# Performance work log

Hardware: AMD Instinct MI355X
Metric: run time of the kernel (lower is better)

The kernel has to match this reference:

```python
import jax, jax.numpy as jnp
import numpy as np

NUM_PRODUCTS = 100000
NUM_CATEGORIES = 1000
P_DIM = 64          # product embedding dim
C_DIM = P_DIM // 2  # 32
T_DIM = P_DIM // 4  # 16
U_DIM = P_DIM // 4  # 16
HID = 128
B, S, L = 1024, 50, 20


def setup_inputs() -> dict:
    key = jax.random.key(0)
    ks = jax.random.split(key, 24)
    inp = {}
    inp['product_input'] = jax.random.randint(ks[0], (B, S, L), 1, NUM_PRODUCTS + 1, dtype=jnp.int32)
    inp['categories_input'] = jax.random.randint(ks[1], (B, S, L), 1, NUM_CATEGORIES + 1, dtype=jnp.int32)
    inp['user_age_input'] = jax.random.uniform(ks[2], (B,), jnp.float32) * 80.0
    inp['user_timestamps_input'] = jax.random.uniform(ks[3], (B, S), jnp.float32)
    inp['user_gender_input'] = jax.random.randint(ks[4], (B,), 0, 2).astype(jnp.float32)
    # embedding tables (padding_idx=0 -> zero row)
    emb_p = jax.random.normal(ks[5], (NUM_PRODUCTS + 1, P_DIM), jnp.float32) * 0.02
    inp['emb_p'] = emb_p.at[0].set(0.0)
    emb_c = jax.random.normal(ks[6], (NUM_CATEGORIES + 1, C_DIM), jnp.float32) * 0.02
    inp['emb_c'] = emb_c.at[0].set(0.0)
    # small linears
    inp['W_ts'] = jax.random.normal(ks[7], (T_DIM, 1), jnp.float32) * 0.1
    inp['b_ts'] = jnp.zeros((T_DIM,), jnp.float32)
    inp['W_uf'] = jax.random.normal(ks[8], (U_DIM, 2), jnp.float32) * 0.1
    inp['b_uf'] = jnp.zeros((U_DIM,), jnp.float32)
    # 2-layer LSTM params (torch layout: [4H, in], gate order i,f,g,o)
    IN = P_DIM + C_DIM + T_DIM + U_DIM  # 128
    sc = 1.0 / np.sqrt(HID)
    inp['W_ih0'] = jax.random.uniform(ks[9], (4 * HID, IN), jnp.float32, -sc, sc)
    inp['W_hh0'] = jax.random.uniform(ks[10], (4 * HID, HID), jnp.float32, -sc, sc)
    inp['b_ih0'] = jax.random.uniform(ks[11], (4 * HID,), jnp.float32, -sc, sc)
    inp['b_hh0'] = jax.random.uniform(ks[12], (4 * HID,), jnp.float32, -sc, sc)
    inp['W_ih1'] = jax.random.uniform(ks[13], (4 * HID, HID), jnp.float32, -sc, sc)
    inp['W_hh1'] = jax.random.uniform(ks[14], (4 * HID, HID), jnp.float32, -sc, sc)
    inp['b_ih1'] = jax.random.uniform(ks[15], (4 * HID,), jnp.float32, -sc, sc)
    inp['b_hh1'] = jax.random.uniform(ks[16], (4 * HID,), jnp.float32, -sc, sc)
    # MLP head
    inp['W1'] = jax.random.normal(ks[17], (HID // 2, HID), jnp.float32) * 0.05
    inp['b1'] = jnp.zeros((HID // 2,), jnp.float32)
    inp['W2'] = jax.random.normal(ks[18], (NUM_PRODUCTS + 1, HID // 2), jnp.float32) * 0.05
    inp['b2'] = jnp.zeros((NUM_PRODUCTS + 1,), jnp.float32)
    return inp


def _lstm_layer(x, Wih, Whh, bih, bhh):
    # x: [S, B, D] -> outputs [S, B, H], final h [B, H]
    Bb = x.shape[1]
    h0 = jnp.zeros((Bb, HID), x.dtype)
    def step(carry, xt):
        h, c = carry
        gates = xt @ Wih.T + bih + h @ Whh.T + bhh
        i, f, g, o = jnp.split(gates, 4, axis=-1)
        c = jax.nn.sigmoid(f) * c + jax.nn.sigmoid(i) * jnp.tanh(g)
        h = jax.nn.sigmoid(o) * jnp.tanh(c)
        return (h, c), h
    (h, c), ys = jax.lax.scan(step, (h0, h0), x)
    return ys, h


def reference(product_input, categories_input, user_age_input, user_timestamps_input,
              user_gender_input, emb_p, emb_c, W_ts, b_ts, W_uf, b_uf,
              W_ih0, W_hh0, b_ih0, b_hh0, W_ih1, W_hh1, b_ih1, b_hh1,
              W1, b1, W2, b2):
    # per-basket mean-pooled embeddings (fused gather + segment mean)
    prod = emb_p[product_input].mean(axis=2)          # [B, S, 64]
    cat = emb_c[categories_input].mean(axis=2)        # [B, S, 32]
    ts = user_timestamps_input[..., None] @ W_ts.T + b_ts  # [B, S, 16]
    uf = jnp.stack([user_age_input, user_gender_input], axis=1) @ W_uf.T + b_uf  # [B, 16]
    uf = jnp.broadcast_to(uf[:, None, :], (uf.shape[0], prod.shape[1], uf.shape[1]))
    x = jnp.concatenate([prod, cat, ts, uf], axis=-1)  # [B, S, 128]
    x = jnp.transpose(x, (1, 0, 2))                    # [S, B, 128]
    ys0, _ = _lstm_layer(x, W_ih0, W_hh0, b_ih0, b_hh0)
    _, h_last = _lstm_layer(ys0, W_ih1, W_hh1, b_ih1, b_hh1)  # [B, H]
    # dropout is identity in eval mode
    hidden = jax.nn.relu(h_last @ W1.T + b1)
    logits = hidden @ W2.T + b2                        # [B, num_products+1]
    return logits
```

## Files before the change

### kernel.cpp

```cpp
#include <hip/hip_runtime.h>

#define B_    1024
#define S_    50
#define L_    20
#define NOUT  100001

typedef __attribute__((ext_vector_type(8))) short bh8;
typedef __attribute__((ext_vector_type(4))) float fx4;

__device__ __forceinline__ unsigned short f2bf(float x){
  unsigned u = __float_as_uint(x);
  unsigned r = (u + 0x7FFFu + ((u >> 16) & 1u)) >> 16;
  return (unsigned short)r;
}
__device__ __forceinline__ float bf2f(unsigned short h){
  return __uint_as_float(((unsigned)h) << 16);
}
__device__ __forceinline__ float sigm(float x){
  return __builtin_amdgcn_rcpf(1.f + __expf(-x));
}
__device__ __forceinline__ float tanh_(float x){
  return 1.f - 2.f*__builtin_amdgcn_rcpf(__expf(2.f*x) + 1.f);
}

__device__ __forceinline__ void frag_convert_row(const float* src, bh8& hv, bh8& lv){
  #pragma unroll
  for (int j = 0; j < 8; j++){
    float x = src[j];
    unsigned short hb = f2bf(x);
    hv[j] = (short)hb;
    lv[j] = (short)f2bf(x - bf2f(hb));
  }
}

__global__ __launch_bounds__(256) void prep_lstm_w(
    const float* __restrict__ Wih0, const float* __restrict__ Whh0,
    const float* __restrict__ bih0, const float* __restrict__ bhh0,
    const float* __restrict__ Wih1, const float* __restrict__ Whh1,
    const float* __restrict__ bih1, const float* __restrict__ bhh1,
    short* __restrict__ wsw, float* __restrict__ wsbias){
  int tid = blockIdx.x*256 + threadIdx.x;
  if (tid < 1024){
    int l = tid >> 9, n = tid & 511;
    wsbias[l*512 + n] = l ? (bih1[n] + bhh1[n]) : (bih0[n] + bhh0[n]);
  }
  if (tid >= 32768) return;
  int lane = tid & 63;
  int kt   = (tid >> 6) & 7;
  int nt   = (tid >> 9) & 31;
  int l    = tid >> 14;
  const float* Wih = l ? Wih1 : Wih0;
  const float* Whh = l ? Whh1 : Whh0;
  int n = nt*16 + (lane & 15);
  int kbase = kt*32 + (lane >> 4)*8;
  size_t base = ((((size_t)l*32 + nt)*8 + kt)*64 + lane)*8;
  for (int j = 0; j < 8; j++){
    int k = kbase + j;
    float w = (k < 128) ? Wih[n*128 + k] : Whh[n*128 + (k - 128)];
    wsw[base + j] = (short)f2bf(w);
  }
}

__global__ __launch_bounds__(256) void prep_w2(const float* __restrict__ W2,
                                               short* __restrict__ out){
  long i = (long)blockIdx.x*256 + threadIdx.x;
  if (i >= 100016L*64) return;
  long row = i >> 6;
  float v = (row < NOUT) ? W2[i] : 0.f;
  out[i] = (short)f2bf(v);
}

__global__ __launch_bounds__(256) void features(
    const int* __restrict__ pidx, const int* __restrict__ cidx,
    const float* __restrict__ age, const float* __restrict__ ts,
    const float* __restrict__ gender,
    const float* __restrict__ embp, const float* __restrict__ embc,
    const float* __restrict__ Wts, const float* __restrict__ bts,
    const float* __restrict__ Wuf, const float* __restrict__ bufv,
    short* __restrict__ xfrag){
  const int bx = blockIdx.x;
  const int bt = bx & 63, s = bx >> 6;
  const int b0 = bt*16;
  const int tid = threadIdx.x;
  __shared__ int pi[320], ci[320];
  __shared__ __align__(16) float XF[16][132];
  for (int i = tid; i < 640; i += 256){
    if (i < 320){
      int row = i/20, l = i - row*20;
      pi[i] = pidx[((size_t)(b0+row)*S_ + s)*L_ + l];
    } else {
      int j = i - 320;
      int row = j/20, l = j - row*20;
      ci[j] = cidx[((size_t)(b0+row)*S_ + s)*L_ + l];
    }
  }
  __syncthreads();
  const int m = tid >> 4, fg = tid & 15;
  float a[8];
  if (fg < 8){
    int f0 = fg*8;
    float4 s0 = {0,0,0,0}, s1 = {0,0,0,0};
    for (int l = 0; l < L_; l++){
      const float4* p = (const float4*)(embp + (size_t)pi[m*20+l]*64 + f0);
      float4 u = p[0], v = p[1];
      s0.x += u.x; s0.y += u.y; s0.z += u.z; s0.w += u.w;
      s1.x += v.x; s1.y += v.y; s1.z += v.z; s1.w += v.w;
    }
    a[0]=s0.x*0.05f; a[1]=s0.y*0.05f; a[2]=s0.z*0.05f; a[3]=s0.w*0.05f;
    a[4]=s1.x*0.05f; a[5]=s1.y*0.05f; a[6]=s1.z*0.05f; a[7]=s1.w*0.05f;
  } else if (fg < 12){
    int f0 = (fg-8)*8;
    float4 s0 = {0,0,0,0}, s1 = {0,0,0,0};
    for (int l = 0; l < L_; l++){
      const float4* p = (const float4*)(embc + (size_t)ci[m*20+l]*32 + f0);
      float4 u = p[0], v = p[1];
      s0.x += u.x; s0.y += u.y; s0.z += u.z; s0.w += u.w;
      s1.x += v.x; s1.y += v.y; s1.z += v.z; s1.w += v.w;
    }
    a[0]=s0.x*0.05f; a[1]=s0.y*0.05f; a[2]=s0.z*0.05f; a[3]=s0.w*0.05f;
    a[4]=s1.x*0.05f; a[5]=s1.y*0.05f; a[6]=s1.z*0.05f; a[7]=s1.w*0.05f;
  } else if (fg < 14){
    int j0 = (fg-12)*8;
    float tv = ts[(size_t)(b0+m)*S_ + s];
    #pragma unroll
    for (int e = 0; e < 8; e++) a[e] = tv*Wts[j0+e] + bts[j0+e];
  } else {
    int j0 = (fg-14)*8;
    float av = age[b0+m], gv = gender[b0+m];
    #pragma unroll
    for (int e = 0; e < 8; e++){
      int j = j0+e;
      a[e] = av*Wuf[2*j] + gv*Wuf[2*j+1] + bufv[j];
    }
  }
  {
    int f0 = fg*8;
    *(float4*)&XF[m][f0]   = (float4){a[0],a[1],a[2],a[3]};
    *(float4*)&XF[m][f0+4] = (float4){a[4],a[5],a[6],a[7]};
  }
  __syncthreads();
  const int kt = tid >> 6, ls = tid & 63;
  const int mm = ls & 15, a2 = ls >> 4;
  bh8 hv, lv;
  frag_convert_row(&XF[mm][kt*32 + a2*8], hv, lv);
  size_t ob = ((((size_t)s*64 + bt)*2 + 0)*4 + kt)*512 + (size_t)ls*8;
  *(bh8*)(xfrag + ob)        = hv;
  *(bh8*)(xfrag + ob + 2048) = lv;
}

__global__ __launch_bounds__(1024, 4) void lstm_kernel(
    const short* __restrict__ xfrag, const short* __restrict__ wsw,
    const float* __restrict__ wsbias,
    const float* __restrict__ W1, const float* __restrict__ b1,
    short* __restrict__ hidden_bf){
  __shared__ __align__(16) short XAhi[2][2048], XAlo[2][2048];
  __shared__ __align__(16) short H0hi[2][2048], H0lo[2][2048];
  __shared__ __align__(16) short H1hi[2][2048], H1lo[2][2048];
  __shared__ __align__(16) float XH0f[16][132], XH1f[16][132];
  const int tid  = threadIdx.x;
  const int w    = tid >> 6, lane = tid & 63;
  const int col  = lane & 15, quad = lane >> 4;
  const int bt   = blockIdx.x;
  const int u    = w & 7;
  const bool t1  = (w >= 8);
  const int lsel = t1 ? 1 : 0;
  const int pl2  = tid >> 9, sl2 = tid & 511;
  const bh8* wp = (const bh8*)wsw;

  for (int idx = tid; idx < 2048; idx += 1024){
    H0hi[1][idx] = 0; H0lo[1][idx] = 0;
    H1hi[0][idx] = 0; H1lo[0][idx] = 0;
  }
  float bz[4];
  #pragma unroll
  for (int g = 0; g < 4; g++)
    bz[g] = wsbias[lsel*512 + (g*8 + u)*16 + col];
  float cst[4] = {0,0,0,0};
  {
    float2 v = *(const float2*)(xfrag + ((size_t)bt*2 + pl2)*2048 + (size_t)sl2*4);
    *(float2*)((pl2 ? XAlo[0] : XAhi[0]) + sl2*4) = v;
  }
  __syncthreads();

  for (int i = 0; i <= S_; i++){
    const int cb = i & 1, pb = cb ^ 1;
    int tp = (i+1 < S_) ? i+1 : S_-1;
    float2 pf = *(const float2*)(xfrag + (((size_t)tp*64 + bt)*2 + pl2)*2048 + (size_t)sl2*4);

    const bool act = t1 ? (i >= 1) : (i < S_);
    if (act){
      fx4 acc[4];
      #pragma unroll
      for (int g = 0; g < 4; g++)
        acc[g] = (fx4){bz[g], bz[g], bz[g], bz[g]};
      __builtin_amdgcn_s_setprio(1);
      #pragma unroll
      for (int kt = 0; kt < 8; kt++){
        const short* ph;
        const short* pl;
        if (!t1){
          ph = (kt < 4) ? &XAhi[cb][kt*512 + lane*8] : &H0hi[pb][(kt-4)*512 + lane*8];
          pl = (kt < 4) ? &XAlo[cb][kt*512 + lane*8] : &H0lo[pb][(kt-4)*512 + lane*8];
        } else {
          ph = (kt < 4) ? &H0hi[pb][kt*512 + lane*8] : &H1hi[pb][(kt-4)*512 + lane*8];
          pl = (kt < 4) ? &H0lo[pb][kt*512 + lane*8] : &H1lo[pb][(kt-4)*512 + lane*8];
        }
        bh8 ah = *(const bh8*)ph;
        bh8 al = *(const bh8*)pl;
        #pragma unroll
        for (int g = 0; g < 4; g++){
          bh8 bb = wp[(size_t)((lsel*32 + g*8 + u)*8 + kt)*64 + lane];
          acc[g] = __builtin_amdgcn_mfma_f32_16x16x32_bf16(ah, bb, acc[g], 0, 0, 0);
          acc[g] = __builtin_amdgcn_mfma_f32_16x16x32_bf16(al, bb, acc[g], 0, 0, 0);
        }
      }
      __builtin_amdgcn_s_setprio(0);
      float (*XH)[132] = t1 ? XH1f : XH0f;
      #pragma unroll
      for (int r = 0; r < 4; r++){
        float cc = sigm(acc[1][r])*cst[r] + sigm(acc[0][r])*tanh_(acc[2][r]);
        cst[r] = cc;
        XH[quad*4 + r][u*16 + col] = sigm(acc[3][r])*tanh_(cc);
      }
      {
        const int mm = lane & 15, qq = (lane >> 4) & 1, phase = lane >> 5;
        bh8 hv, lv;
        frag_convert_row(&XH[mm][u*16 + qq*8], hv, lv);
        const int off = (u >> 1)*512 + ((2*(u & 1) + qq)*16 + mm)*8;
        short* dsth = t1 ? &H1hi[cb][off] : &H0hi[cb][off];
        short* dstl = t1 ? &H1lo[cb][off] : &H0lo[cb][off];
        short* dst  = phase ? dstl : dsth;
        bh8   val   = phase ? lv : hv;
        *(bh8*)dst = val;
      }
    }
    *(float2*)((pl2 ? XAlo[pb] : XAhi[pb]) + sl2*4) = pf;
    __syncthreads();
  }
  {
    const int mm2 = tid >> 6;
    const int cc2 = tid & 63;
    float s = b1[cc2];
    #pragma unroll 8
    for (int k = 0; k < 128; k++) s += XH1f[mm2][k]*W1[cc2*128 + k];
    s = fmaxf(s, 0.f);
    hidden_bf[(size_t)(bt*16 + mm2)*64 + cc2] = (short)f2bf(s);
  }
}

__global__ __launch_bounds__(256) void head2(
    const short* __restrict__ hid, const short* __restrict__ w2,
    const float* __restrict__ b2, float* __restrict__ out){
  __shared__ __align__(16) float HS[4][16][132];
  const int tid = threadIdx.x;
  const int w = tid >> 6, lane = tid & 63;
  const int col = lane & 15, quad = lane >> 4;
  const int mt = blockIdx.x & 63;
  const int chunk = blockIdx.x >> 6;
  const bh8* hp = (const bh8*)hid;
  bh8 a0 = hp[(size_t)(mt*16 + col)*8 + quad];
  bh8 a1 = hp[(size_t)(mt*16 + col)*8 + 4 + quad];
  const bh8* wpt = (const bh8*)w2;
  #pragma unroll
  for (int i = 0; i < 8; i++){
    int nt = chunk*32 + w*8 + i;
    if (nt < 6251){
      int n = nt*16 + col;
      bh8 b0v = wpt[(size_t)n*8 + quad];
      bh8 b1v = wpt[(size_t)n*8 + 4 + quad];
      fx4 a = {0.f,0.f,0.f,0.f};
      a = __builtin_amdgcn_mfma_f32_16x16x32_bf16(a0, b0v, a, 0, 0, 0);
      a = __builtin_amdgcn_mfma_f32_16x16x32_bf16(a1, b1v, a, 0, 0, 0);
      float bias = (n < NOUT) ? b2[n] : 0.f;
      #pragma unroll
      for (int r = 0; r < 4; r++) HS[w][quad*4 + r][i*16 + col] = a[r] + bias;
    }
  }
  __syncthreads();
  const long rowbase = (long)mt*16;
  const int n0 = chunk*512 + w*128;
  #pragma unroll
  for (int p = 0; p < 8; p++){
    int row = p*2 + (lane >> 5);
    int c4 = (lane & 31)*4;
    int gc = n0 + c4;
    float4 v = *(const float4*)&HS[w][row][c4];
    if (gc + 3 < NOUT){
      *(float4*)&out[(rowbase + row)*NOUT + gc] = v;
    } else {
      float vv[4] = {v.x, v.y, v.z, v.w};
      #pragma unroll
      for (int k2 = 0; k2 < 4; k2++)
        if (gc + k2 < NOUT) out[(rowbase + row)*NOUT + gc + k2] = vv[k2];
    }
  }
}

extern "C" void kernel_launch(void* const* d_in, const int* in_sizes, int n_in,
                              void* d_out, int out_size, void* d_ws, size_t ws_size,
                              hipStream_t stream){
  const int*   prod = (const int*)  d_in[0];
  const int*   cat  = (const int*)  d_in[1];
  const float* age  = (const float*)d_in[2];
  const float* ts   = (const float*)d_in[3];
  const float* gen  = (const float*)d_in[4];
  const float* embp = (const float*)d_in[5];
  const float* embc = (const float*)d_in[6];
  const float* Wts  = (const float*)d_in[7];
  const float* bts  = (const float*)d_in[8];
  const float* Wuf  = (const float*)d_in[9];
  const float* bufv = (const float*)d_in[10];
  const float* Wih0 = (const float*)d_in[11];
  const float* Whh0 = (const float*)d_in[12];
  const float* bih0 = (const float*)d_in[13];
  const float* bhh0 = (const float*)d_in[14];
  const float* Wih1 = (const float*)d_in[15];
  const float* Whh1 = (const float*)d_in[16];
  const float* bih1 = (const float*)d_in[17];
  const float* bhh1 = (const float*)d_in[18];
  const float* W1   = (const float*)d_in[19];
  const float* b1   = (const float*)d_in[20];
  const float* W2   = (const float*)d_in[21];
  const float* b2   = (const float*)d_in[22];
  float* out = (float*)d_out;

  char* ws = (char*)d_ws;
  short* ws_x    = (short*)(ws);
  short* ws_w    = (short*)(ws + 26214400);
  float* ws_bias = (float*)(ws + 26738688);
  short* ws_hid  = (short*)(ws + 26742784);
  short* ws_w2   = (short*)(ws + 26873856);

  prep_lstm_w<<<128, 256, 0, stream>>>(Wih0, Whh0, bih0, bhh0,
                                       Wih1, Whh1, bih1, bhh1, ws_w, ws_bias);
  prep_w2<<<25004, 256, 0, stream>>>(W2, ws_w2);
  features<<<3200, 256, 0, stream>>>(prod, cat, age, ts, gen, embp, embc,
                                     Wts, bts, Wuf, bufv, ws_x);
  lstm_kernel<<<64, 1024, 0, stream>>>(ws_x, ws_w, ws_bias, W1, b1, ws_hid);
  head2<<<196*64, 256, 0, stream>>>(ws_hid, ws_w2, b2, out);
}
```

Measured before the change: 983.5 us.

## Keep LSTM recurrent weights resident in registers and LDS; swizzle head block order

The LSTM kernel previously reloaded every weight fragment from global memory on each of the 51 timesteps. It now pins 14 fragments per wave in VGPRs and 5 in an added LDS pool. The remaining fragments are streamed from global memory, with their loads spread across the unrolled MFMA sequence to hide latency. The head2 kernel remaps block indices with an XCD-style swizzle to improve L2 locality for W2 and the hidden rows. In exchange, register and LDS pressure rise sharply (an extra 80KB of LDS per block), which may cause spills or lower occupancy.

New measurement: 1.039 ms. +5.6%, slower.

```diff
diff --git a/kernel.cpp b/kernel.cpp
--- a/kernel.cpp
+++ b/kernel.cpp
@@ -157,6 +157,7 @@
   __shared__ __align__(16) short H0hi[2][2048], H0lo[2][2048];
   __shared__ __align__(16) short H1hi[2][2048], H1lo[2][2048];
   __shared__ __align__(16) float XH0f[16][132], XH1f[16][132];
+  __shared__ __align__(16) short WPOOL[40960];
   const int tid  = threadIdx.x;
   const int w    = tid >> 6, lane = tid & 63;
   const int col  = lane & 15, quad = lane >> 4;
@@ -167,6 +168,9 @@
   const int pl2  = tid >> 9, sl2 = tid & 511;
   const bh8* wp = (const bh8*)wsw;
 
+#define WF(g,kt) wp[((size_t)((lsel*32 + (g)*8 + u)*8 + (kt))*64) + lane]
+#define PW(kt)   (*(const bh8*)&WPOOL[((w*5 + (kt))*64 + lane)*8])
+
   for (int idx = tid; idx < 2048; idx += 1024){
     H0hi[1][idx] = 0; H0lo[1][idx] = 0;
     H1hi[0][idx] = 0; H1lo[0][idx] = 0;
@@ -176,6 +180,19 @@
   for (int g = 0; g < 4; g++)
     bz[g] = wsbias[lsel*512 + (g*8 + u)*16 + col];
   float cst[4] = {0,0,0,0};
+
+  bh8 wr0[7], wr1[7];
+  #pragma unroll
+  for (int kt = 0; kt < 7; kt++){
+    wr0[kt] = WF(0, kt);
+    wr1[kt] = WF(1, kt);
+  }
+  #pragma unroll
+  for (int p = 0; p < 5; p++){
+    bh8 v = WF(2, p);
+    *(bh8*)&WPOOL[((w*5 + p)*64 + lane)*8] = v;
+  }
+
   {
     float2 v = *(const float2*)(xfrag + ((size_t)bt*2 + pl2)*2048 + (size_t)sl2*4);
     *(float2*)((pl2 ? XAlo[0] : XAhi[0]) + sl2*4) = v;
@@ -193,28 +210,33 @@
       #pragma unroll
       for (int g = 0; g < 4; g++)
         acc[g] = (fx4){bz[g], bz[g], bz[g], bz[g]};
+      bh8 ah, al;
+#define AFRAG(kt) { \
+      const short* ph_; const short* pl_; \
+      if (!t1){ ph_ = ((kt) < 4) ? &XAhi[cb][(kt)*512 + lane*8] : &H0hi[pb][((kt)-4)*512 + lane*8]; \
+                pl_ = ((kt) < 4) ? &XAlo[cb][(kt)*512 + lane*8] : &H0lo[pb][((kt)-4)*512 + lane*8]; } \
+      else    { ph_ = ((kt) < 4) ? &H0hi[pb][(kt)*512 + lane*8] : &H1hi[pb][((kt)-4)*512 + lane*8]; \
+                pl_ = ((kt) < 4) ? &H0lo[pb][(kt)*512 + lane*8] : &H1lo[pb][((kt)-4)*512 + lane*8]; } \
+      ah = *(const bh8*)ph_; al = *(const bh8*)pl_; }
+#define MM(g, W) \
+      acc[g] = __builtin_amdgcn_mfma_f32_16x16x32_bf16(ah, (W), acc[g], 0, 0, 0); \
+      acc[g] = __builtin_amdgcn_mfma_f32_16x16x32_bf16(al, (W), acc[g], 0, 0, 0);
+
+      bh8 s30 = WF(3,0), s31 = WF(3,1), s32 = WF(3,2), s33 = WF(3,3);
       __builtin_amdgcn_s_setprio(1);
-      #pragma unroll
-      for (int kt = 0; kt < 8; kt++){
-        const short* ph;
-        const short* pl;
-        if (!t1){
-          ph = (kt < 4) ? &XAhi[cb][kt*512 + lane*8] : &H0hi[pb][(kt-4)*512 + lane*8];
-          pl = (kt < 4) ? &XAlo[cb][kt*512 + lane*8] : &H0lo[pb][(kt-4)*512 + lane*8];
-        } else {
-          ph = (kt < 4) ? &H0hi[pb][kt*512 + lane*8] : &H1hi[pb][(kt-4)*512 + lane*8];
-          pl = (kt < 4) ? &H0lo[pb][kt*512 + lane*8] : &H1lo[pb][(kt-4)*512 + lane*8];
-        }
-        bh8 ah = *(const bh8*)ph;
-        bh8 al = *(const bh8*)pl;
-        #pragma unroll
-        for (int g = 0; g < 4; g++){
-          bh8 bb = wp[(size_t)((lsel*32 + g*8 + u)*8 + kt)*64 + lane];
-          acc[g] = __builtin_amdgcn_mfma_f32_16x16x32_bf16(ah, bb, acc[g], 0, 0, 0);
-          acc[g] = __builtin_amdgcn_mfma_f32_16x16x32_bf16(al, bb, acc[g], 0, 0, 0);
-        }
-      }
+      AFRAG(0); MM(0, wr0[0]); MM(1, wr1[0]); MM(2, PW(0)); MM(3, s30);
+      AFRAG(1); MM(0, wr0[1]); MM(1, wr1[1]); MM(2, PW(1)); MM(3, s31);
+      bh8 s34 = WF(3,4), s35 = WF(3,5), s25 = WF(2,5);
+      AFRAG(2); MM(0, wr0[2]); MM(1, wr1[2]); MM(2, PW(2)); MM(3, s32);
+      AFRAG(3); MM(0, wr0[3]); MM(1, wr1[3]); MM(2, PW(3)); MM(3, s33);
+      bh8 s26 = WF(2,6), s36 = WF(3,6);
+      AFRAG(4); MM(0, wr0[4]); MM(1, wr1[4]); MM(2, PW(4)); MM(3, s34);
+      bh8 s27 = WF(2,7), s37 = WF(3,7), s07 = WF(0,7), s17 = WF(1,7);
+      AFRAG(5); MM(0, wr0[5]); MM(1, wr1[5]); MM(2, s25); MM(3, s35);
+      AFRAG(6); MM(0, wr0[6]); MM(1, wr1[6]); MM(2, s26); MM(3, s36);
+      AFRAG(7); MM(0, s07);    MM(1, s17);    MM(2, s27); MM(3, s37);
       __builtin_amdgcn_s_setprio(0);
+
       float (*XH)[132] = t1 ? XH1f : XH0f;
       #pragma unroll
       for (int r = 0; r < 4; r++){
@@ -246,6 +268,10 @@
     s = fmaxf(s, 0.f);
     hidden_bf[(size_t)(bt*16 + mm2)*64 + cc2] = (short)f2bf(s);
   }
+#undef WF
+#undef PW
+#undef AFRAG
+#undef MM
 }
 
 __global__ __launch_bounds__(256) void head2(
@@ -255,8 +281,10 @@
   const int tid = threadIdx.x;
   const int w = tid >> 6, lane = tid & 63;
   const int col = lane & 15, quad = lane >> 4;
-  const int mt = blockIdx.x & 63;
-  const int chunk = blockIdx.x >> 6;
+  const int bsw = blockIdx.x;
+  const int wg  = (bsw & 7)*1568 + (bsw >> 3);
+  const int mt = wg & 63;
+  const int chunk = wg >> 6;
   const bh8* hp = (const bh8*)hid;
   bh8 a0 = hp[(size_t)(mt*16 + col)*8 + quad];
   bh8 a1 = hp[(size_t)(mt*16 + col)*8 + 4 + quad];
```

## Precompute layer-0 input gates in a parallel kernel before the recurrent LSTM

Applied to the files above, without the earlier changes.

Adds a pregate0 kernel that computes the layer-0 input projection (W_ih0·x + bias) for all timesteps in parallel across 3200 blocks and stores it in fp32 workspace. The recurrent kernel then only does the hidden-state matmul for layer 0, preloading the next step's pregates while computing the current one. It also stages part of the layer-1 weights in shared memory and keeps more in registers. This removes input-projection MFMAs from the serial critical path, at the cost of about 100MB of extra global memory traffic. The new path is used only when the workspace is large enough, otherwise it falls back to the legacy kernel.

New measurement: 1.019 ms. +3.6%, slower.

```diff
diff --git a/kernel.cpp b/kernel.cpp
--- a/kernel.cpp
+++ b/kernel.cpp
@@ -148,7 +148,205 @@
   *(bh8*)(xfrag + ob + 2048) = lv;
 }
 
-__global__ __launch_bounds__(1024, 4) void lstm_kernel(
+__global__ __launch_bounds__(256) void pregate0(
+    const short* __restrict__ xfrag, const short* __restrict__ wsw,
+    const float* __restrict__ wsbias, float* __restrict__ pg){
+  const int bx = blockIdx.x;
+  const int bt = bx & 63, s = bx >> 6;
+  const int tid = threadIdx.x;
+  const int wv = tid >> 6, lane = tid & 63;
+  const int col = lane & 15;
+  const bh8* wp = (const bh8*)wsw;
+  bh8 ah[4], al[4];
+  #pragma unroll
+  for (int kt = 0; kt < 4; kt++){
+    size_t ob = ((((size_t)s*64 + bt)*2 + 0)*4 + kt)*512 + (size_t)lane*8;
+    ah[kt] = *(const bh8*)(xfrag + ob);
+    al[kt] = *(const bh8*)(xfrag + ob + 2048);
+  }
+  fx4* pgout = (fx4*)pg;
+  #pragma unroll
+  for (int e = 0; e < 2; e++){
+    const int uu = wv*2 + e;
+    #pragma unroll
+    for (int g = 0; g < 4; g++){
+      float bzv = wsbias[(g*8 + uu)*16 + col];
+      fx4 acc = (fx4){bzv, bzv, bzv, bzv};
+      #pragma unroll
+      for (int kt = 0; kt < 4; kt++){
+        bh8 bb = wp[(size_t)((g*8 + uu)*8 + kt)*64 + lane];
+        acc = __builtin_amdgcn_mfma_f32_16x16x32_bf16(ah[kt], bb, acc, 0, 0, 0);
+        acc = __builtin_amdgcn_mfma_f32_16x16x32_bf16(al[kt], bb, acc, 0, 0, 0);
+      }
+      pgout[((((size_t)s*64 + bt)*8 + uu)*4 + g)*64 + lane] = acc;
+    }
+  }
+}
+
+__global__ __launch_bounds__(1024, 4) void lstm_pre(
+    const float* __restrict__ pg0, const short* __restrict__ wsw,
+    const float* __restrict__ wsbias,
+    const float* __restrict__ W1, const float* __restrict__ b1,
+    short* __restrict__ hidden_bf){
+  __shared__ __align__(16) short H0hi[2][2048], H0lo[2][2048];
+  __shared__ __align__(16) short H1hi[2][2048], H1lo[2][2048];
+  __shared__ __align__(16) float XH0f[16][132], XH1f[16][132];
+  __shared__ __align__(16) short WPOOL[32768];
+  const int tid  = threadIdx.x;
+  const int w    = tid >> 6, lane = tid & 63;
+  const int col  = lane & 15, quad = lane >> 4;
+  const int bt   = blockIdx.x;
+  const int u    = w & 7;
+  const bool t1  = (w >= 8);
+  const bh8* wp = (const bh8*)wsw;
+  const fx4* pgp = (const fx4*)pg0;
+
+#define WFL(l,g,kt) wp[((size_t)(((l)*32 + (g)*8 + u)*8 + (kt))*64) + lane]
+#define PWP(kt)     (*(const bh8*)&WPOOL[((u*8 + (kt))*64 + lane)*8])
+
+  for (int idx = tid; idx < 2048; idx += 1024){
+    H0hi[1][idx] = 0; H0lo[1][idx] = 0;
+    H1hi[0][idx] = 0; H1lo[0][idx] = 0;
+  }
+  float bz[4] = {0,0,0,0};
+  if (t1){
+    #pragma unroll
+    for (int g = 0; g < 4; g++)
+      bz[g] = wsbias[512 + (g*8 + u)*16 + col];
+  }
+  float cst[4] = {0,0,0,0};
+
+  bh8 wpin[16];
+  if (!t1){
+    #pragma unroll
+    for (int g = 0; g < 4; g++)
+      #pragma unroll
+      for (int k4 = 0; k4 < 4; k4++)
+        wpin[g*4 + k4] = WFL(0, g, 4 + k4);
+  } else {
+    #pragma unroll
+    for (int g = 0; g < 2; g++)
+      #pragma unroll
+      for (int kt = 0; kt < 8; kt++)
+        wpin[g*8 + kt] = WFL(1, g, kt);
+    #pragma unroll
+    for (int kt = 0; kt < 8; kt++){
+      bh8 v = WFL(1, 2, kt);
+      *(bh8*)&WPOOL[((u*8 + kt)*64 + lane)*8] = v;
+    }
+  }
+  #pragma unroll
+  for (int q = 0; q < 16; q++) asm volatile("" : "+v"(wpin[q]));
+
+  fx4 pgv[4];
+  if (!t1){
+    #pragma unroll
+    for (int g = 0; g < 4; g++)
+      pgv[g] = pgp[((((size_t)0*64 + bt)*8 + u)*4 + g)*64 + lane];
+  }
+  __syncthreads();
+
+#define MM2(g, W) \
+      acc[g] = __builtin_amdgcn_mfma_f32_16x16x32_bf16(ah, (W), acc[g], 0, 0, 0); \
+      acc[g] = __builtin_amdgcn_mfma_f32_16x16x32_bf16(al, (W), acc[g], 0, 0, 0);
+
+  for (int i = 0; i <= S_; i++){
+    const int cb = i & 1, pb = cb ^ 1;
+    if (!t1){
+      if (i < S_){
+        fx4 acc[4];
+        #pragma unroll
+        for (int g = 0; g < 4; g++) acc[g] = pgv[g];
+        if (i + 1 < S_){
+          #pragma unroll
+          for (int g = 0; g < 4; g++)
+            pgv[g] = pgp[((((size_t)(i+1)*64 + bt)*8 + u)*4 + g)*64 + lane];
+        }
+        bh8 ah, al;
+        __builtin_amdgcn_s_setprio(1);
+        #pragma unroll
+        for (int k4 = 0; k4 < 4; k4++){
+          ah = *(const bh8*)&H0hi[pb][k4*512 + lane*8];
+          al = *(const bh8*)&H0lo[pb][k4*512 + lane*8];
+          MM2(0, wpin[0*4 + k4]); MM2(1, wpin[1*4 + k4]);
+          MM2(2, wpin[2*4 + k4]); MM2(3, wpin[3*4 + k4]);
+        }
+        __builtin_amdgcn_s_setprio(0);
+        #pragma unroll
+        for (int r = 0; r < 4; r++){
+          float cc = sigm(acc[1][r])*cst[r] + sigm(acc[0][r])*tanh_(acc[2][r]);
+          cst[r] = cc;
+          XH0f[quad*4 + r][u*16 + col] = sigm(acc[3][r])*tanh_(cc);
+        }
+        {
+          const int mm = lane & 15, qq = (lane >> 4) & 1, phase = lane >> 5;
+          bh8 hv, lv;
+          frag_convert_row(&XH0f[mm][u*16 + qq*8], hv, lv);
+          const int off = (u >> 1)*512 + ((2*(u & 1) + qq)*16 + mm)*8;
+          short* dst = phase ? &H0lo[cb][off] : &H0hi[cb][off];
+          bh8 val = phase ? lv : hv;
+          *(bh8*)dst = val;
+        }
+      }
+    } else {
+      if (i >= 1){
+        fx4 acc[4];
+        #pragma unroll
+        for (int g = 0; g < 4; g++)
+          acc[g] = (fx4){bz[g], bz[g], bz[g], bz[g]};
+        bh8 ah, al;
+        bh8 s30 = WFL(1,3,0), s31 = WFL(1,3,1), s32 = WFL(1,3,2), s33 = WFL(1,3,3);
+        __builtin_amdgcn_s_setprio(1);
+        #pragma unroll
+        for (int kt = 0; kt < 4; kt++){
+          ah = *(const bh8*)&H0hi[pb][kt*512 + lane*8];
+          al = *(const bh8*)&H0lo[pb][kt*512 + lane*8];
+          bh8 s3 = (kt==0)?s30:(kt==1)?s31:(kt==2)?s32:s33;
+          MM2(0, wpin[kt]); MM2(1, wpin[8 + kt]); MM2(2, PWP(kt)); MM2(3, s3);
+        }
+        bh8 s34 = WFL(1,3,4), s35 = WFL(1,3,5), s36 = WFL(1,3,6), s37 = WFL(1,3,7);
+        #pragma unroll
+        for (int k4 = 0; k4 < 4; k4++){
+          ah = *(const bh8*)&H1hi[pb][k4*512 + lane*8];
+          al = *(const bh8*)&H1lo[pb][k4*512 + lane*8];
+          bh8 s3 = (k4==0)?s34:(k4==1)?s35:(k4==2)?s36:s37;
+          MM2(0, wpin[4 + k4]); MM2(1, wpin[12 + k4]); MM2(2, PWP(4 + k4)); MM2(3, s3);
+        }
+        __builtin_amdgcn_s_setprio(0);
+        #pragma unroll
+        for (int r = 0; r < 4; r++){
+          float cc = sigm(acc[1][r])*cst[r] + sigm(acc[0][r])*tanh_(acc[2][r]);
+          cst[r] = cc;
+          XH1f[quad*4 + r][u*16 + col] = sigm(acc[3][r])*tanh_(cc);
+        }
+        {
+          const int mm = lane & 15, qq = (lane >> 4) & 1, phase = lane >> 5;
+          bh8 hv, lv;
+          frag_convert_row(&XH1f[mm][u*16 + qq*8], hv, lv);
+          const int off = (u >> 1)*512 + ((2*(u & 1) + qq)*16 + mm)*8;
+          short* dst = phase ? &H1lo[cb][off] : &H1hi[cb][off];
+          bh8 val = phase ? lv : hv;
+          *(bh8*)dst = val;
+        }
+      }
+    }
+    __syncthreads();
+  }
+  {
+    const int mm2 = tid >> 6;
+    const int cc2 = tid & 63;
+    float s = b1[cc2];
+    #pragma unroll 8
+    for (int k = 0; k < 128; k++) s += XH1f[mm2][k]*W1[cc2*128 + k];
+    s = fmaxf(s, 0.f);
+    hidden_bf[(size_t)(bt*16 + mm2)*64 + cc2] = (short)f2bf(s);
+  }
+#undef WFL
+#undef PWP
+#undef MM2
+}
+
+__global__ __launch_bounds__(1024, 4) void lstm_legacy(
     const short* __restrict__ xfrag, const short* __restrict__ wsw,
     const float* __restrict__ wsbias,
     const float* __restrict__ W1, const float* __restrict__ b1,
@@ -330,12 +528,20 @@
   float* ws_bias = (float*)(ws + 26738688);
   short* ws_hid  = (short*)(ws + 26742784);
   short* ws_w2   = (short*)(ws + 26873856);
+  float* ws_pg   = (float*)(ws + 39675904);
+  const size_t PRE_NEED = 39675904ULL + 104857600ULL;
+  const bool pre = (ws_size >= PRE_NEED);
 
   prep_lstm_w<<<128, 256, 0, stream>>>(Wih0, Whh0, bih0, bhh0,
                                        Wih1, Whh1, bih1, bhh1, ws_w, ws_bias);
   prep_w2<<<25004, 256, 0, stream>>>(W2, ws_w2);
   features<<<3200, 256, 0, stream>>>(prod, cat, age, ts, gen, embp, embc,
                                      Wts, bts, Wuf, bufv, ws_x);
-  lstm_kernel<<<64, 1024, 0, stream>>>(ws_x, ws_w, ws_bias, W1, b1, ws_hid);
+  if (pre){
+    pregate0<<<3200, 256, 0, stream>>>(ws_x, ws_w, ws_bias, ws_pg);
+    lstm_pre<<<64, 1024, 0, stream>>>(ws_pg, ws_w, ws_bias, W1, b1, ws_hid);
+  } else {
+    lstm_legacy<<<64, 1024, 0, stream>>>(ws_x, ws_w, ws_bias, W1, b1, ws_hid);
+  }
   head2<<<196*64, 256, 0, stream>>>(ws_hid, ws_w2, b2, out);
 }
```
